# Kernel tuning notes

Measured on AMD Instinct MI355X. Metric: run time of the kernel, lower is better.

## Reference

```python
import jax, jax.numpy as jnp
import numpy as np

EPS = 1e-8
LN_EPS = 1e-5
TOPK_FEAT = 5

def _extract_features(p):
    # p: [B, E, C] probability posteriors
    logp = jnp.log(p + EPS)
    ent = -jnp.sum(p * logp, axis=-1)                      # [B,E] entropy
    tk = jax.lax.top_k(p, TOPK_FEAT)[0]                    # [B,E,5]
    topk_mass = jnp.sum(tk, axis=-1)                       # [B,E]
    residual = 1.0 - topk_mass
    max_probs = tk[..., 0]                                 # top-1 == max
    top_gap = tk[..., 0] - tk[..., 1]
    mean_p = jnp.mean(p, axis=1, keepdims=True)            # [B,1,C]
    # cosine similarity to ensemble mean (F.cosine_similarity, eps=1e-8)
    dot = jnp.sum(p * mean_p, axis=-1)                     # [B,E]
    pn = jnp.maximum(jnp.linalg.norm(p, axis=-1), EPS)
    mn = jnp.maximum(jnp.linalg.norm(mean_p, axis=-1), EPS)  # [B,1]
    cos = dot / (pn * mn)
    kl = jnp.sum(p * (logp - jnp.log(mean_p + EPS)), axis=-1)  # [B,E]
    mp = mean_p[:, 0, :]                                   # [B,C]
    mean_ent = -jnp.sum(mp * jnp.log(mp + EPS), axis=-1)   # [B]
    class_var = jnp.var(p, axis=1, ddof=1)                 # [B,C] unbiased (torch default)
    mean_class_var = jnp.mean(class_var, axis=-1)          # [B]
    std_max = jnp.std(max_probs, axis=-1, ddof=1)          # [B]
    per_expert = jnp.concatenate(
        [ent, topk_mass, residual, max_probs, top_gap, cos, kl], axis=1)  # [B,7E]
    glob = jnp.stack([mean_ent, mean_class_var, std_max], axis=1)          # [B,3]
    feats = jnp.concatenate([per_expert, glob], axis=1)
    return jnp.clip(feats, -100.0, 100.0)

def _layernorm(x, g, b):
    mu = jnp.mean(x, axis=-1, keepdims=True)
    var = jnp.mean((x - mu) ** 2, axis=-1, keepdims=True)
    return (x - mu) / jnp.sqrt(var + LN_EPS) * g + b

def setup_inputs() -> dict:
    key = jax.random.key(0)
    ks = jax.random.split(key, 8)
    B, E, C = 16384, 8, 1000
    D, H1, H2 = 7 * E + 3, 256, 128
    posteriors = jax.nn.softmax(jax.random.normal(ks[0], (B, E, C), jnp.float32), axis=-1)
    def xavier(k, fi, fo):
        lim = np.sqrt(6.0 / (fi + fo))
        return jax.random.uniform(k, (fi, fo), jnp.float32, -lim, lim)
    return {
        "posteriors": posteriors,
        "W1": xavier(ks[1], D, H1), "b1": jnp.zeros((H1,), jnp.float32),
        "g1": jnp.ones((H1,), jnp.float32), "beta1": jnp.zeros((H1,), jnp.float32),
        "W2": xavier(ks[2], H1, H2), "b2": jnp.zeros((H2,), jnp.float32),
        "g2": jnp.ones((H2,), jnp.float32), "beta2": jnp.zeros((H2,), jnp.float32),
        "W3": xavier(ks[3], H2, E), "b3": jnp.zeros((E,), jnp.float32),
    }

def reference(posteriors, W1, b1, g1, beta1, W2, b2, g2, beta2, W3, b3):
    # feature extractor is @torch.no_grad in the original
    feats = jax.lax.stop_gradient(_extract_features(posteriors))  # [B, 7E+3]
    h = jax.nn.relu(_layernorm(feats @ W1 + b1, g1, beta1))       # dropout off (eval)
    h = jax.nn.relu(_layernorm(h @ W2 + b2, g2, beta2))
    logits = h @ W3 + b3                                          # [B, E]
    weights = jax.nn.softmax(logits, axis=-1)                     # dense routing
    return weights, logits, feats
```

## Files before the change

### kernel.cpp

```cpp
#include <hip/hip_runtime.h>
#include <hip/hip_bf16.h>
#include <math.h>

#define EXP_E 8
#define NCLS 1000
#define DFEAT 59
#define EPSF 1e-8f
#define LN_EPSF 1e-5f

__device__ __forceinline__ float wave_allsum(float v) {
#pragma unroll
  for (int m = 32; m; m >>= 1) v += __shfl_xor(v, m, 64);
  return v;
}

__device__ __forceinline__ float half_allsum(float v) {
#pragma unroll
  for (int m = 16; m; m >>= 1) v += __shfl_xor(v, m, 64);
  return v;
}

#define INS5(px)                                            \
  {                                                         \
    float x_ = (px), m_;                                    \
    m_ = fmaxf(t0, x_); x_ = fminf(t0, x_); t0 = m_;        \
    m_ = fmaxf(t1, x_); x_ = fminf(t1, x_); t1 = m_;        \
    m_ = fmaxf(t2, x_); x_ = fminf(t2, x_); t2 = m_;        \
    m_ = fmaxf(t3, x_); x_ = fminf(t3, x_); t3 = m_;        \
    t4 = fmaxf(t4, x_);                                     \
  }

#define ACCUM(pv, mv, lmv)                                  \
  {                                                         \
    float p_ = (pv);                                        \
    float lp_ = __logf(p_ + EPSF);                          \
    ent += p_ * lp_;                                        \
    sq += p_ * p_;                                          \
    dot += p_ * (mv);                                       \
    kl += p_ * (lp_ - (lmv));                               \
    INS5(p_);                                               \
  }

__global__ __launch_bounds__(256) void feat_kernel(const float* __restrict__ post,
                                                   float* __restrict__ fout) {
  __shared__ float sp[EXP_E * NCLS];
  __shared__ float smp[NCLS];
  __shared__ float slmp[NCLS];
  __shared__ float sred[12];
  __shared__ float sfeat[DFEAT];

  const int tid = threadIdx.x;
  const int b = blockIdx.x;
  const float* pb = post + (size_t)b * (EXP_E * NCLS);

  const float4* pb4 = reinterpret_cast<const float4*>(pb);
  float4* sp4 = reinterpret_cast<float4*>(sp);
  for (int i = tid; i < (EXP_E * NCLS) / 4; i += 256) sp4[i] = pb4[i];
  __syncthreads();

  float a_ment = 0.f, a_mvar = 0.f, a_mn2 = 0.f;
  if (tid < 250) {
    const int c4 = tid * 4;
    float vv[EXP_E][4];
#pragma unroll
    for (int e2 = 0; e2 < EXP_E; ++e2) {
      float4 t = *reinterpret_cast<const float4*>(sp + e2 * NCLS + c4);
      vv[e2][0] = t.x; vv[e2][1] = t.y; vv[e2][2] = t.z; vv[e2][3] = t.w;
    }
    float mpv[4], lmv[4];
#pragma unroll
    for (int j = 0; j < 4; ++j) {
      float s1 = 0.f;
#pragma unroll
      for (int e2 = 0; e2 < EXP_E; ++e2) s1 += vv[e2][j];
      float mp = s1 * 0.125f;
      float q = 0.f;
#pragma unroll
      for (int e2 = 0; e2 < EXP_E; ++e2) { float d = vv[e2][j] - mp; q += d * d; }
      a_mvar += q * (1.f / 7.f);
      float lmp = __logf(mp + EPSF);
      mpv[j] = mp; lmv[j] = lmp;
      a_ment += mp * lmp;
      a_mn2 += mp * mp;
    }
    *reinterpret_cast<float4*>(smp + c4)  = make_float4(mpv[0], mpv[1], mpv[2], mpv[3]);
    *reinterpret_cast<float4*>(slmp + c4) = make_float4(lmv[0], lmv[1], lmv[2], lmv[3]);
  }
  a_ment = wave_allsum(a_ment);
  a_mvar = wave_allsum(a_mvar);
  a_mn2 = wave_allsum(a_mn2);
  const int wv = tid >> 6;
  if ((tid & 63) == 0) {
    sred[wv * 3 + 0] = a_ment;
    sred[wv * 3 + 1] = a_mvar;
    sred[wv * 3 + 2] = a_mn2;
  }
  __syncthreads();
  const float s_ment = sred[0] + sred[3] + sred[6] + sred[9];
  const float s_mvar = sred[1] + sred[4] + sred[7] + sred[10];
  const float s_mn2  = sred[2] + sred[5] + sred[8] + sred[11];
  const float mn = fmaxf(sqrtf(s_mn2), EPSF);

  const int e = tid >> 5;
  const int l32 = tid & 31;
  float ent = 0.f, sq = 0.f, dot = 0.f, kl = 0.f;
  float t0 = -1.f, t1 = -1.f, t2 = -1.f, t3 = -1.f, t4 = -1.f;
  const float4* spe4 = reinterpret_cast<const float4*>(sp + e * NCLS);
  const float4* smp4 = reinterpret_cast<const float4*>(smp);
  const float4* slm4 = reinterpret_cast<const float4*>(slmp);
  for (int k = l32; k < 250; k += 32) {
    float4 p4 = spe4[k];
    float4 m4 = smp4[k];
    float4 l4 = slm4[k];
    ACCUM(p4.x, m4.x, l4.x);
    ACCUM(p4.y, m4.y, l4.y);
    ACCUM(p4.z, m4.z, l4.z);
    ACCUM(p4.w, m4.w, l4.w);
  }
  ent = half_allsum(ent);
  sq  = half_allsum(sq);
  dot = half_allsum(dot);
  kl  = half_allsum(kl);
#pragma unroll
  for (int m = 1; m <= 16; m <<= 1) {
    float o0 = __shfl_xor(t0, m, 64), o1 = __shfl_xor(t1, m, 64), o2 = __shfl_xor(t2, m, 64),
          o3 = __shfl_xor(t3, m, 64), o4 = __shfl_xor(t4, m, 64);
    float r0 = fmaxf(t0, o0);
    float r1 = fmaxf(fmaxf(t1, o1), fminf(t0, o0));
    float r2 = fmaxf(fmaxf(t2, o2), fmaxf(fminf(t1, o0), fminf(t0, o1)));
    float r3 = fmaxf(fmaxf(t3, o3),
                     fmaxf(fminf(t2, o0), fmaxf(fminf(t1, o1), fminf(t0, o2))));
    float r4 = fmaxf(fmaxf(t4, o4),
                     fmaxf(fmaxf(fminf(t3, o0), fminf(t2, o1)),
                           fmaxf(fminf(t1, o2), fminf(t0, o3))));
    t0 = r0; t1 = r1; t2 = r2; t3 = r3; t4 = r4;
  }

  if (l32 == 0) {
    float mass = t0 + t1 + t2 + t3 + t4;
    float pn = fmaxf(sqrtf(sq), EPSF);
    sfeat[0 * 8 + e] = -ent;
    sfeat[1 * 8 + e] = mass;
    sfeat[2 * 8 + e] = 1.f - mass;
    sfeat[3 * 8 + e] = t0;
    sfeat[4 * 8 + e] = t0 - t1;
    sfeat[5 * 8 + e] = dot / (pn * mn);
    sfeat[6 * 8 + e] = kl;
  }
  __syncthreads();
  if (tid == 0) {
    float s = 0.f;
#pragma unroll
    for (int i = 0; i < 8; ++i) s += sfeat[24 + i];
    float mu = s * 0.125f;
    float q = 0.f;
#pragma unroll
    for (int i = 0; i < 8; ++i) { float d = sfeat[24 + i] - mu; q += d * d; }
    sfeat[56] = -s_ment;
    sfeat[57] = s_mvar * (1.f / (float)NCLS);
    sfeat[58] = sqrtf(q * (1.f / 7.f));
  }
  __syncthreads();
  if (tid < DFEAT) {
    float v = sfeat[tid];
    v = fminf(fmaxf(v, -100.f), 100.f);
    fout[(size_t)b * DFEAT + tid] = v;
  }
}

__global__ __launch_bounds__(256) void mlp_kernel(
    const float* __restrict__ feats,
    const float* __restrict__ W1, const float* __restrict__ b1,
    const float* __restrict__ g1, const float* __restrict__ be1,
    const float* __restrict__ W2, const float* __restrict__ b2,
    const float* __restrict__ g2, const float* __restrict__ be2,
    const float* __restrict__ W3, const float* __restrict__ b3,
    float* __restrict__ out_w, float* __restrict__ out_l) {
  __shared__ float sfe[32 * DFEAT];
  __shared__ float h1[32 * 256];
  __shared__ float h2[32 * 132];
  __shared__ float sW3[128 * 8];

  const int tid = threadIdx.x;
  const int r0 = blockIdx.x * 32;

  {
    const float4* f4 = reinterpret_cast<const float4*>(feats + (size_t)r0 * DFEAT);
    float4* s4 = reinterpret_cast<float4*>(sfe);
    for (int i = tid; i < (32 * DFEAT) / 4; i += 256) s4[i] = f4[i];
    const float4* w4 = reinterpret_cast<const float4*>(W3);
    float4* sw4 = reinterpret_cast<float4*>(sW3);
    if (tid < 256) sw4[tid] = w4[tid];
  }
  __syncthreads();

  float acc[32];
#pragma unroll
  for (int r = 0; r < 32; ++r) acc[r] = 0.f;
  for (int k = 0; k < DFEAT; ++k) {
    float w = W1[k * 256 + tid];
#pragma unroll
    for (int r = 0; r < 32; ++r) acc[r] += sfe[r * DFEAT + k] * w;
  }
  {
    float bb = b1[tid];
#pragma unroll
    for (int r = 0; r < 32; ++r) h1[r * 256 + tid] = acc[r] + bb;
  }
  __syncthreads();

  const int wvi = tid >> 6, ln = tid & 63;
  for (int rr = 0; rr < 8; ++rr) {
    int r = wvi * 8 + rr;
    float x0 = h1[r * 256 + ln],        x1 = h1[r * 256 + ln + 64];
    float x2 = h1[r * 256 + ln + 128],  x3 = h1[r * 256 + ln + 192];
    float s = wave_allsum(x0 + x1 + x2 + x3);
    float mu = s * (1.f / 256.f);
    float d0 = x0 - mu, d1 = x1 - mu, d2 = x2 - mu, d3 = x3 - mu;
    float q = wave_allsum(d0 * d0 + d1 * d1 + d2 * d2 + d3 * d3);
    float inv = 1.0f / sqrtf(q * (1.f / 256.f) + LN_EPSF);
    h1[r * 256 + ln]       = fmaxf(d0 * inv * g1[ln]       + be1[ln],       0.f);
    h1[r * 256 + ln + 64]  = fmaxf(d1 * inv * g1[ln + 64]  + be1[ln + 64],  0.f);
    h1[r * 256 + ln + 128] = fmaxf(d2 * inv * g1[ln + 128] + be1[ln + 128], 0.f);
    h1[r * 256 + ln + 192] = fmaxf(d3 * inv * g1[ln + 192] + be1[ln + 192], 0.f);
  }
  __syncthreads();

  const int j2 = tid & 127, rh = tid >> 7;
  float a2[16];
#pragma unroll
  for (int r = 0; r < 16; ++r) a2[r] = 0.f;
  for (int k = 0; k < 256; ++k) {
    float w = W2[k * 128 + j2];
#pragma unroll
    for (int r = 0; r < 16; ++r) a2[r] += h1[(rh * 16 + r) * 256 + k] * w;
  }
  {
    float bb = b2[j2];
#pragma unroll
    for (int r = 0; r < 16; ++r) h2[(rh * 16 + r) * 132 + j2] = a2[r] + bb;
  }
  __syncthreads();

  for (int rr = 0; rr < 8; ++rr) {
    int r = wvi * 8 + rr;
    float x0 = h2[r * 132 + ln], x1 = h2[r * 132 + ln + 64];
    float s = wave_allsum(x0 + x1);
    float mu = s * (1.f / 128.f);
    float d0 = x0 - mu, d1 = x1 - mu;
    float q = wave_allsum(d0 * d0 + d1 * d1);
    float inv = 1.0f / sqrtf(q * (1.f / 128.f) + LN_EPSF);
    h2[r * 132 + ln]      = fmaxf(d0 * inv * g2[ln]      + be2[ln],      0.f);
    h2[r * 132 + ln + 64] = fmaxf(d1 * inv * g2[ln + 64] + be2[ln + 64], 0.f);
  }
  __syncthreads();

  {
    const int r = tid >> 3, e = tid & 7;
    float s = b3[e];
    for (int k = 0; k < 128; ++k) s += h2[r * 132 + k] * sW3[k * 8 + e];
    float m = s;
#pragma unroll
    for (int mk = 4; mk; mk >>= 1) m = fmaxf(m, __shfl_xor(m, mk, 64));
    float ex = __expf(s - m);
    float den = ex;
#pragma unroll
    for (int mk = 4; mk; mk >>= 1) den += __shfl_xor(den, mk, 64);
    out_l[(size_t)(r0 + r) * 8 + e] = s;
    out_w[(size_t)(r0 + r) * 8 + e] = ex / den;
  }
}

extern "C" void kernel_launch(void* const* d_in, const int* in_sizes, int n_in,
                              void* d_out, int out_size, void* d_ws, size_t ws_size,
                              hipStream_t stream) {
  const float* post = (const float*)d_in[0];
  const float* W1  = (const float*)d_in[1];
  const float* b1  = (const float*)d_in[2];
  const float* g1  = (const float*)d_in[3];
  const float* be1 = (const float*)d_in[4];
  const float* W2  = (const float*)d_in[5];
  const float* b2  = (const float*)d_in[6];
  const float* g2  = (const float*)d_in[7];
  const float* be2 = (const float*)d_in[8];
  const float* W3  = (const float*)d_in[9];
  const float* b3  = (const float*)d_in[10];

  float* out = (float*)d_out;
  const int B = in_sizes[0] / (EXP_E * NCLS);

  float* out_w = out;
  float* out_l = out + (size_t)B * 8;
  float* fout  = out + (size_t)2 * B * 8;

  hipLaunchKernelGGL(feat_kernel, dim3(B), dim3(256), 0, stream, post, fout);
  hipLaunchKernelGGL(mlp_kernel, dim3(B / 32), dim3(256), 0, stream,
                     fout, W1, b1, g1, be1, W2, b2, g2, be2, W3, b3, out_w, out_l);
}
```

Baseline: 780.4 us.

## Widen feature kernel to 512 threads and register-tile MLP with fused layernorm

Result: no change. 786.0 us (+0.7%).

```diff
diff --git a/kernel.cpp b/kernel.cpp
--- a/kernel.cpp
+++ b/kernel.cpp
@@ -34,42 +34,40 @@
   {                                                         \
     float p_ = (pv);                                        \
     float lp_ = __logf(p_ + EPSF);                          \
-    ent += p_ * lp_;                                        \
+    splogp += p_ * lp_;                                     \
     sq += p_ * p_;                                          \
     dot += p_ * (mv);                                       \
-    kl += p_ * (lp_ - (lmv));                               \
+    splmp += p_ * (lmv);                                    \
     INS5(p_);                                               \
   }
 
-__global__ __launch_bounds__(256) void feat_kernel(const float* __restrict__ post,
-                                                   float* __restrict__ fout) {
-  __shared__ float sp[EXP_E * NCLS];
-  __shared__ float smp[NCLS];
-  __shared__ float slmp[NCLS];
-  __shared__ float sred[12];
+__global__ __launch_bounds__(512, 4) void feat_kernel(const float* __restrict__ post,
+                                                      float* __restrict__ fout) {
+  __shared__ __align__(16) float sp[EXP_E * NCLS];
+  __shared__ __align__(16) float smp[NCLS];
+  __shared__ __align__(16) float slmp[NCLS];
+  __shared__ float sred[24];
   __shared__ float sfeat[DFEAT];
 
   const int tid = threadIdx.x;
   const int b = blockIdx.x;
   const float* pb = post + (size_t)b * (EXP_E * NCLS);
 
-  const float4* pb4 = reinterpret_cast<const float4*>(pb);
-  float4* sp4 = reinterpret_cast<float4*>(sp);
-  for (int i = tid; i < (EXP_E * NCLS) / 4; i += 256) sp4[i] = pb4[i];
-  __syncthreads();
-
   float a_ment = 0.f, a_mvar = 0.f, a_mn2 = 0.f;
-  if (tid < 250) {
-    const int c4 = tid * 4;
-    float vv[EXP_E][4];
-#pragma unroll
-    for (int e2 = 0; e2 < EXP_E; ++e2) {
-      float4 t = *reinterpret_cast<const float4*>(sp + e2 * NCLS + c4);
-      vv[e2][0] = t.x; vv[e2][1] = t.y; vv[e2][2] = t.z; vv[e2][3] = t.w;
-    }
-    float mpv[4], lmv[4];
-#pragma unroll
-    for (int j = 0; j < 4; ++j) {
+  if (tid < 500) {
+    const float2* pb2 = reinterpret_cast<const float2*>(pb);
+    float2 v[EXP_E];
+#pragma unroll
+    for (int e2 = 0; e2 < EXP_E; ++e2) v[e2] = pb2[e2 * 500 + tid];
+    float2* sp2 = reinterpret_cast<float2*>(sp);
+#pragma unroll
+    for (int e2 = 0; e2 < EXP_E; ++e2) sp2[e2 * 500 + tid] = v[e2];
+    float vv[EXP_E][2];
+#pragma unroll
+    for (int e2 = 0; e2 < EXP_E; ++e2) { vv[e2][0] = v[e2].x; vv[e2][1] = v[e2].y; }
+    float mpj[2], lmj[2];
+#pragma unroll
+    for (int j = 0; j < 2; ++j) {
       float s1 = 0.f;
 #pragma unroll
       for (int e2 = 0; e2 < EXP_E; ++e2) s1 += vv[e2][j];
@@ -79,12 +77,12 @@
       for (int e2 = 0; e2 < EXP_E; ++e2) { float d = vv[e2][j] - mp; q += d * d; }
       a_mvar += q * (1.f / 7.f);
       float lmp = __logf(mp + EPSF);
-      mpv[j] = mp; lmv[j] = lmp;
       a_ment += mp * lmp;
       a_mn2 += mp * mp;
-    }
-    *reinterpret_cast<float4*>(smp + c4)  = make_float4(mpv[0], mpv[1], mpv[2], mpv[3]);
-    *reinterpret_cast<float4*>(slmp + c4) = make_float4(lmv[0], lmv[1], lmv[2], lmv[3]);
+      mpj[j] = mp; lmj[j] = lmp;
+    }
+    reinterpret_cast<float2*>(smp)[tid]  = make_float2(mpj[0], mpj[1]);
+    reinterpret_cast<float2*>(slmp)[tid] = make_float2(lmj[0], lmj[1]);
   }
   a_ment = wave_allsum(a_ment);
   a_mvar = wave_allsum(a_mvar);
@@ -96,19 +94,23 @@
     sred[wv * 3 + 2] = a_mn2;
   }
   __syncthreads();
-  const float s_ment = sred[0] + sred[3] + sred[6] + sred[9];
-  const float s_mvar = sred[1] + sred[4] + sred[7] + sred[10];
-  const float s_mn2  = sred[2] + sred[5] + sred[8] + sred[11];
+  float s_ment = 0.f, s_mvar = 0.f, s_mn2 = 0.f;
+#pragma unroll
+  for (int w = 0; w < 8; ++w) {
+    s_ment += sred[w * 3 + 0];
+    s_mvar += sred[w * 3 + 1];
+    s_mn2  += sred[w * 3 + 2];
+  }
   const float mn = fmaxf(sqrtf(s_mn2), EPSF);
 
-  const int e = tid >> 5;
-  const int l32 = tid & 31;
-  float ent = 0.f, sq = 0.f, dot = 0.f, kl = 0.f;
+  const int e = tid >> 6;
+  const int lane = tid & 63;
+  float splogp = 0.f, sq = 0.f, dot = 0.f, splmp = 0.f;
   float t0 = -1.f, t1 = -1.f, t2 = -1.f, t3 = -1.f, t4 = -1.f;
   const float4* spe4 = reinterpret_cast<const float4*>(sp + e * NCLS);
   const float4* smp4 = reinterpret_cast<const float4*>(smp);
   const float4* slm4 = reinterpret_cast<const float4*>(slmp);
-  for (int k = l32; k < 250; k += 32) {
+  for (int k = lane; k < 250; k += 64) {
     float4 p4 = spe4[k];
     float4 m4 = smp4[k];
     float4 l4 = slm4[k];
@@ -117,12 +119,12 @@
     ACCUM(p4.z, m4.z, l4.z);
     ACCUM(p4.w, m4.w, l4.w);
   }
-  ent = half_allsum(ent);
-  sq  = half_allsum(sq);
-  dot = half_allsum(dot);
-  kl  = half_allsum(kl);
-#pragma unroll
-  for (int m = 1; m <= 16; m <<= 1) {
+  splogp = wave_allsum(splogp);
+  sq     = wave_allsum(sq);
+  dot    = wave_allsum(dot);
+  splmp  = wave_allsum(splmp);
+#pragma unroll
+  for (int m = 1; m <= 32; m <<= 1) {
     float o0 = __shfl_xor(t0, m, 64), o1 = __shfl_xor(t1, m, 64), o2 = __shfl_xor(t2, m, 64),
           o3 = __shfl_xor(t3, m, 64), o4 = __shfl_xor(t4, m, 64);
     float r0 = fmaxf(t0, o0);
@@ -136,16 +138,16 @@
     t0 = r0; t1 = r1; t2 = r2; t3 = r3; t4 = r4;
   }
 
-  if (l32 == 0) {
+  if (lane == 0) {
     float mass = t0 + t1 + t2 + t3 + t4;
     float pn = fmaxf(sqrtf(sq), EPSF);
-    sfeat[0 * 8 + e] = -ent;
+    sfeat[0 * 8 + e] = -splogp;
     sfeat[1 * 8 + e] = mass;
     sfeat[2 * 8 + e] = 1.f - mass;
     sfeat[3 * 8 + e] = t0;
     sfeat[4 * 8 + e] = t0 - t1;
     sfeat[5 * 8 + e] = dot / (pn * mn);
-    sfeat[6 * 8 + e] = kl;
+    sfeat[6 * 8 + e] = splogp - splmp;
   }
   __syncthreads();
   if (tid == 0) {
@@ -176,89 +178,129 @@
     const float* __restrict__ g2, const float* __restrict__ be2,
     const float* __restrict__ W3, const float* __restrict__ b3,
     float* __restrict__ out_w, float* __restrict__ out_l) {
-  __shared__ float sfe[32 * DFEAT];
-  __shared__ float h1[32 * 256];
-  __shared__ float h2[32 * 132];
-  __shared__ float sW3[128 * 8];
+  __shared__ __align__(16) float sfe[32 * 60];
+  __shared__ __align__(16) float h1T[256 * 36];
+  __shared__ __align__(16) float h2[32 * 132];
+  __shared__ __align__(16) float sW3[128 * 8];
 
   const int tid = threadIdx.x;
   const int r0 = blockIdx.x * 32;
 
-  {
-    const float4* f4 = reinterpret_cast<const float4*>(feats + (size_t)r0 * DFEAT);
-    float4* s4 = reinterpret_cast<float4*>(sfe);
-    for (int i = tid; i < (32 * DFEAT) / 4; i += 256) s4[i] = f4[i];
-    const float4* w4 = reinterpret_cast<const float4*>(W3);
-    float4* sw4 = reinterpret_cast<float4*>(sW3);
-    if (tid < 256) sw4[tid] = w4[tid];
-  }
-  __syncthreads();
-
-  float acc[32];
-#pragma unroll
-  for (int r = 0; r < 32; ++r) acc[r] = 0.f;
+  for (int i = tid; i < 32 * DFEAT; i += 256) {
+    int r = i / DFEAT;
+    int k = i - r * DFEAT;
+    sfe[r * 60 + k] = feats[(size_t)r0 * DFEAT + i];
+  }
+  reinterpret_cast<float4*>(sW3)[tid] = reinterpret_cast<const float4*>(W3)[tid];
+  __syncthreads();
+
+  const int cg = tid & 63, rg = tid >> 6;
+  float acc[4][8];
+#pragma unroll
+  for (int c = 0; c < 4; ++c)
+#pragma unroll
+    for (int r = 0; r < 8; ++r) acc[c][r] = 0.f;
   for (int k = 0; k < DFEAT; ++k) {
-    float w = W1[k * 256 + tid];
-#pragma unroll
-    for (int r = 0; r < 32; ++r) acc[r] += sfe[r * DFEAT + k] * w;
-  }
-  {
-    float bb = b1[tid];
-#pragma unroll
-    for (int r = 0; r < 32; ++r) h1[r * 256 + tid] = acc[r] + bb;
-  }
-  __syncthreads();
-
-  const int wvi = tid >> 6, ln = tid & 63;
-  for (int rr = 0; rr < 8; ++rr) {
-    int r = wvi * 8 + rr;
-    float x0 = h1[r * 256 + ln],        x1 = h1[r * 256 + ln + 64];
-    float x2 = h1[r * 256 + ln + 128],  x3 = h1[r * 256 + ln + 192];
-    float s = wave_allsum(x0 + x1 + x2 + x3);
-    float mu = s * (1.f / 256.f);
-    float d0 = x0 - mu, d1 = x1 - mu, d2 = x2 - mu, d3 = x3 - mu;
-    float q = wave_allsum(d0 * d0 + d1 * d1 + d2 * d2 + d3 * d3);
-    float inv = 1.0f / sqrtf(q * (1.f / 256.f) + LN_EPSF);
-    h1[r * 256 + ln]       = fmaxf(d0 * inv * g1[ln]       + be1[ln],       0.f);
-    h1[r * 256 + ln + 64]  = fmaxf(d1 * inv * g1[ln + 64]  + be1[ln + 64],  0.f);
-    h1[r * 256 + ln + 128] = fmaxf(d2 * inv * g1[ln + 128] + be1[ln + 128], 0.f);
-    h1[r * 256 + ln + 192] = fmaxf(d3 * inv * g1[ln + 192] + be1[ln + 192], 0.f);
-  }
-  __syncthreads();
-
-  const int j2 = tid & 127, rh = tid >> 7;
-  float a2[16];
-#pragma unroll
-  for (int r = 0; r < 16; ++r) a2[r] = 0.f;
+    float4 w = *reinterpret_cast<const float4*>(W1 + k * 256 + cg * 4);
+    float s[8];
+#pragma unroll
+    for (int r = 0; r < 8; ++r) s[r] = sfe[(rg * 8 + r) * 60 + k];
+#pragma unroll
+    for (int r = 0; r < 8; ++r) {
+      acc[0][r] += s[r] * w.x;
+      acc[1][r] += s[r] * w.y;
+      acc[2][r] += s[r] * w.z;
+      acc[3][r] += s[r] * w.w;
+    }
+  }
+  {
+    float4 bb = *reinterpret_cast<const float4*>(b1 + cg * 4);
+#pragma unroll
+    for (int r = 0; r < 8; ++r) {
+      acc[0][r] += bb.x; acc[1][r] += bb.y; acc[2][r] += bb.z; acc[3][r] += bb.w;
+    }
+  }
+  {
+    float4 gg = *reinterpret_cast<const float4*>(g1 + cg * 4);
+    float4 ee = *reinterpret_cast<const float4*>(be1 + cg * 4);
+#pragma unroll
+    for (int r = 0; r < 8; ++r) {
+      float sum = wave_allsum(acc[0][r] + acc[1][r] + acc[2][r] + acc[3][r]);
+      float mu = sum * (1.f / 256.f);
+      float d0 = acc[0][r] - mu, d1 = acc[1][r] - mu, d2 = acc[2][r] - mu, d3 = acc[3][r] - mu;
+      float q = wave_allsum(d0 * d0 + d1 * d1 + d2 * d2 + d3 * d3);
+      float inv = 1.0f / sqrtf(q * (1.f / 256.f) + LN_EPSF);
+      acc[0][r] = fmaxf(d0 * inv * gg.x + ee.x, 0.f);
+      acc[1][r] = fmaxf(d1 * inv * gg.y + ee.y, 0.f);
+      acc[2][r] = fmaxf(d2 * inv * gg.z + ee.z, 0.f);
+      acc[3][r] = fmaxf(d3 * inv * gg.w + ee.w, 0.f);
+    }
+  }
+#pragma unroll
+  for (int c = 0; c < 4; ++c) {
+    float* dst = h1T + (cg * 4 + c) * 36 + rg * 8;
+    *reinterpret_cast<float4*>(dst)     = make_float4(acc[c][0], acc[c][1], acc[c][2], acc[c][3]);
+    *reinterpret_cast<float4*>(dst + 4) = make_float4(acc[c][4], acc[c][5], acc[c][6], acc[c][7]);
+  }
+  __syncthreads();
+
+  const int cg2 = tid & 31, rg2 = tid >> 5;
+  float a2[4][4];
+#pragma unroll
+  for (int c = 0; c < 4; ++c)
+#pragma unroll
+    for (int r = 0; r < 4; ++r) a2[c][r] = 0.f;
   for (int k = 0; k < 256; ++k) {
-    float w = W2[k * 128 + j2];
-#pragma unroll
-    for (int r = 0; r < 16; ++r) a2[r] += h1[(rh * 16 + r) * 256 + k] * w;
-  }
-  {
-    float bb = b2[j2];
-#pragma unroll
-    for (int r = 0; r < 16; ++r) h2[(rh * 16 + r) * 132 + j2] = a2[r] + bb;
-  }
-  __syncthreads();
-
-  for (int rr = 0; rr < 8; ++rr) {
-    int r = wvi * 8 + rr;
-    float x0 = h2[r * 132 + ln], x1 = h2[r * 132 + ln + 64];
-    float s = wave_allsum(x0 + x1);
-    float mu = s * (1.f / 128.f);
-    float d0 = x0 - mu, d1 = x1 - mu;
-    float q = wave_allsum(d0 * d0 + d1 * d1);
-    float inv = 1.0f / sqrtf(q * (1.f / 128.f) + LN_EPSF);
-    h2[r * 132 + ln]      = fmaxf(d0 * inv * g2[ln]      + be2[ln],      0.f);
-    h2[r * 132 + ln + 64] = fmaxf(d1 * inv * g2[ln + 64] + be2[ln + 64], 0.f);
-  }
+    float4 h = *reinterpret_cast<const float4*>(h1T + k * 36 + rg2 * 4);
+    float4 w = *reinterpret_cast<const float4*>(W2 + k * 128 + cg2 * 4);
+    float hr[4] = {h.x, h.y, h.z, h.w};
+    float wc[4] = {w.x, w.y, w.z, w.w};
+#pragma unroll
+    for (int c = 0; c < 4; ++c)
+#pragma unroll
+      for (int r = 0; r < 4; ++r) a2[c][r] += hr[r] * wc[c];
+  }
+  {
+    float4 bb = *reinterpret_cast<const float4*>(b2 + cg2 * 4);
+#pragma unroll
+    for (int r = 0; r < 4; ++r) {
+      a2[0][r] += bb.x; a2[1][r] += bb.y; a2[2][r] += bb.z; a2[3][r] += bb.w;
+    }
+  }
+  {
+    float4 gg = *reinterpret_cast<const float4*>(g2 + cg2 * 4);
+    float4 ee = *reinterpret_cast<const float4*>(be2 + cg2 * 4);
+#pragma unroll
+    for (int r = 0; r < 4; ++r) {
+      float sum = half_allsum(a2[0][r] + a2[1][r] + a2[2][r] + a2[3][r]);
+      float mu = sum * (1.f / 128.f);
+      float d0 = a2[0][r] - mu, d1 = a2[1][r] - mu, d2 = a2[2][r] - mu, d3 = a2[3][r] - mu;
+      float q = half_allsum(d0 * d0 + d1 * d1 + d2 * d2 + d3 * d3);
+      float inv = 1.0f / sqrtf(q * (1.f / 128.f) + LN_EPSF);
+      a2[0][r] = fmaxf(d0 * inv * gg.x + ee.x, 0.f);
+      a2[1][r] = fmaxf(d1 * inv * gg.y + ee.y, 0.f);
+      a2[2][r] = fmaxf(d2 * inv * gg.z + ee.z, 0.f);
+      a2[3][r] = fmaxf(d3 * inv * gg.w + ee.w, 0.f);
+    }
+  }
+#pragma unroll
+  for (int r = 0; r < 4; ++r)
+    *reinterpret_cast<float4*>(h2 + (rg2 * 4 + r) * 132 + cg2 * 4) =
+        make_float4(a2[0][r], a2[1][r], a2[2][r], a2[3][r]);
   __syncthreads();
 
   {
     const int r = tid >> 3, e = tid & 7;
     float s = b3[e];
-    for (int k = 0; k < 128; ++k) s += h2[r * 132 + k] * sW3[k * 8 + e];
+    const float4* hrow = reinterpret_cast<const float4*>(h2 + r * 132);
+#pragma unroll
+    for (int k4 = 0; k4 < 32; ++k4) {
+      float4 h = hrow[k4];
+      s += h.x * sW3[(k4 * 4 + 0) * 8 + e];
+      s += h.y * sW3[(k4 * 4 + 1) * 8 + e];
+      s += h.z * sW3[(k4 * 4 + 2) * 8 + e];
+      s += h.w * sW3[(k4 * 4 + 3) * 8 + e];
+    }
     float m = s;
 #pragma unroll
     for (int mk = 4; mk; mk >>= 1) m = fmaxf(m, __shfl_xor(m, mk, 64));
@@ -293,7 +335,7 @@
   float* out_l = out + (size_t)B * 8;
   float* fout  = out + (size_t)2 * B * 8;
 
-  hipLaunchKernelGGL(feat_kernel, dim3(B), dim3(256), 0, stream, post, fout);
+  hipLaunchKernelGGL(feat_kernel, dim3(B), dim3(512), 0, stream, post, fout);
   hipLaunchKernelGGL(mlp_kernel, dim3(B / 32), dim3(256), 0, stream,
                      fout, W1, b1, g1, be1, W2, b2, g2, be2, W3, b3, out_w, out_l);
 }
```
